# Kernel tuning notes

Measured on AMD Instinct MI355X. Metric: run time of the kernel, lower is better.

## Reference

```python
import jax, jax.numpy as jnp
import numpy as np

NUM_Q, NUM_P = 8192, 4096


def setup_inputs() -> dict:
    key = jax.random.key(0)
    k1, k2 = jax.random.split(key)
    pred = jax.random.normal(k1, (NUM_Q, NUM_P), dtype=jnp.float32)
    y = jax.random.randint(k2, (NUM_Q, NUM_P), 0, 2, dtype=jnp.int32)
    # guarantee every query has at least one relevant passage (argwhere(y==1) nonempty)
    y = y.at[:, 0].set(1)
    return {"pred": pred, "y": y}


def reference(pred, y):
    # Per row: comparer = min of pred over relevant (y==1) entries.
    # MarginRankingLoss(margin=0, reduction='mean') with target=(y!=1):
    #   target==1 (non-relevant): max(0, -(comparer - pred_j)) = relu(pred_j - min_rlv)
    #   target==0 (relevant):     max(0, 0) = 0
    rlv = (y == 1)
    min_rlv = jnp.min(jnp.where(rlv, pred, jnp.inf), axis=1, keepdims=True)  # [Q,1]
    hinge = jnp.where(rlv, 0.0, jnp.maximum(pred - min_rlv, 0.0))            # [Q,P]
    per_q = hinge.mean(axis=1)                                               # [Q]
    return per_q.mean()
```

## Files before the change

kernel.cpp:

```cpp
#include <hip/hip_runtime.h>
#include <float.h>

#define NUM_Q 8192
#define NUM_P 4096

typedef float  f32x4 __attribute__((ext_vector_type(4)));
typedef int    i32x4 __attribute__((ext_vector_type(4)));

__global__ __launch_bounds__(256)
void mmrl_kernel(const float* __restrict__ pred,
                 const int* __restrict__ y,
                 float* __restrict__ ws) {
    const int row = blockIdx.x;
    const int t = threadIdx.x;

    const f32x4* prow = reinterpret_cast<const f32x4*>(pred + (size_t)row * NUM_P);
    const i32x4* yrow = reinterpret_cast<const i32x4*>(y + (size_t)row * NUM_P);

    i32x4 yv[4];
#pragma unroll
    for (int i = 0; i < 4; ++i) yv[i] = __builtin_nontemporal_load(&yrow[t + 256 * i]);
    f32x4 pv[4];
#pragma unroll
    for (int i = 0; i < 4; ++i) pv[i] = __builtin_nontemporal_load(&prow[t + 256 * i]);

    unsigned int m = 0u;
#pragma unroll
    for (int i = 0; i < 4; ++i) {
        m |= ((unsigned int)(yv[i].x == 1)      ) << (4 * i);
        m |= ((unsigned int)(yv[i].y == 1) << 1 ) << (4 * i);
        m |= ((unsigned int)(yv[i].z == 1) << 2 ) << (4 * i);
        m |= ((unsigned int)(yv[i].w == 1) << 3 ) << (4 * i);
    }

    float lmin = FLT_MAX;
#pragma unroll
    for (int i = 0; i < 4; ++i) {
        lmin = fminf(lmin, (m & (1u << (4 * i)))     ? pv[i].x : FLT_MAX);
        lmin = fminf(lmin, (m & (2u << (4 * i)))     ? pv[i].y : FLT_MAX);
        lmin = fminf(lmin, (m & (4u << (4 * i)))     ? pv[i].z : FLT_MAX);
        lmin = fminf(lmin, (m & (8u << (4 * i)))     ? pv[i].w : FLT_MAX);
    }
#pragma unroll
    for (int off = 32; off > 0; off >>= 1)
        lmin = fminf(lmin, __shfl_xor(lmin, off));

    __shared__ float smin[4];
    __shared__ float ssum[4];
    const int wave = t >> 6;
    if ((t & 63) == 0) smin[wave] = lmin;
    __syncthreads();
    const float rmin = fminf(fminf(smin[0], smin[1]), fminf(smin[2], smin[3]));

    float lsum = 0.0f;
#pragma unroll
    for (int i = 0; i < 4; ++i) {
        lsum += (m & (1u << (4 * i))) ? 0.0f : fmaxf(pv[i].x - rmin, 0.0f);
        lsum += (m & (2u << (4 * i))) ? 0.0f : fmaxf(pv[i].y - rmin, 0.0f);
        lsum += (m & (4u << (4 * i))) ? 0.0f : fmaxf(pv[i].z - rmin, 0.0f);
        lsum += (m & (8u << (4 * i))) ? 0.0f : fmaxf(pv[i].w - rmin, 0.0f);
    }
#pragma unroll
    for (int off = 32; off > 0; off >>= 1)
        lsum += __shfl_xor(lsum, off);

    if ((t & 63) == 0) ssum[wave] = lsum;
    __syncthreads();

    if (t == 0) {
        ws[row] = (ssum[0] + ssum[1]) + (ssum[2] + ssum[3]);
    }
}

__global__ __launch_bounds__(256)
void mmrl_reduce_kernel(const float* __restrict__ partial,
                        float* __restrict__ out) {
    const int t = threadIdx.x;
    const f32x4* p4 = reinterpret_cast<const f32x4*>(partial);
    float s = 0.0f;
#pragma unroll
    for (int i = 0; i < 8; ++i) {
        f32x4 v = p4[t + 256 * i];
        s += (v.x + v.y) + (v.z + v.w);
    }
#pragma unroll
    for (int off = 32; off > 0; off >>= 1)
        s += __shfl_xor(s, off);

    __shared__ float ss[4];
    if ((t & 63) == 0) ss[t >> 6] = s;
    __syncthreads();

    if (t == 0) {
        const float total = (ss[0] + ss[1]) + (ss[2] + ss[3]);
        out[0] = total * (1.0f / ((float)NUM_Q * (float)NUM_P));
    }
}

extern "C" void kernel_launch(void* const* d_in, const int* in_sizes, int n_in,
                              void* d_out, int out_size, void* d_ws, size_t ws_size,
                              hipStream_t stream) {
    const float* pred = (const float*)d_in[0];
    const int*   y    = (const int*)d_in[1];
    float* out = (float*)d_out;
    float* ws  = (float*)d_ws;

    mmrl_kernel<<<NUM_Q, 256, 0, stream>>>(pred, y, ws);
    mmrl_reduce_kernel<<<1, 256, 0, stream>>>(ws, out);
}
```

Measured before the change: 249.5 us.

## Process two rows per block and write per-wave partial sums

```diff
diff --git a/kernel.cpp b/kernel.cpp
--- a/kernel.cpp
+++ b/kernel.cpp
@@ -11,64 +11,83 @@
 void mmrl_kernel(const float* __restrict__ pred,
                  const int* __restrict__ y,
                  float* __restrict__ ws) {
-    const int row = blockIdx.x;
-    const int t = threadIdx.x;
+    const int row0 = blockIdx.x * 2;
+    const int t    = threadIdx.x;
+    const int wave = t >> 6;
+    const int lane = t & 63;
 
-    const f32x4* prow = reinterpret_cast<const f32x4*>(pred + (size_t)row * NUM_P);
-    const i32x4* yrow = reinterpret_cast<const i32x4*>(y + (size_t)row * NUM_P);
+    const f32x4* p0 = reinterpret_cast<const f32x4*>(pred + (size_t)row0 * NUM_P);
+    const i32x4* y0 = reinterpret_cast<const i32x4*>(y    + (size_t)row0 * NUM_P);
 
-    i32x4 yv[4];
+    i32x4 yv[8];
 #pragma unroll
-    for (int i = 0; i < 4; ++i) yv[i] = __builtin_nontemporal_load(&yrow[t + 256 * i]);
-    f32x4 pv[4];
+    for (int i = 0; i < 4; ++i) yv[i]     = __builtin_nontemporal_load(&y0[t + 256 * i]);
 #pragma unroll
-    for (int i = 0; i < 4; ++i) pv[i] = __builtin_nontemporal_load(&prow[t + 256 * i]);
+    for (int i = 0; i < 4; ++i) yv[4 + i] = __builtin_nontemporal_load(&y0[1024 + t + 256 * i]);
+    f32x4 pv[8];
+#pragma unroll
+    for (int i = 0; i < 4; ++i) pv[i]     = __builtin_nontemporal_load(&p0[t + 256 * i]);
+#pragma unroll
+    for (int i = 0; i < 4; ++i) pv[4 + i] = __builtin_nontemporal_load(&p0[1024 + t + 256 * i]);
 
-    unsigned int m = 0u;
+    unsigned int m0 = 0u, m1 = 0u;
 #pragma unroll
     for (int i = 0; i < 4; ++i) {
-        m |= ((unsigned int)(yv[i].x == 1)      ) << (4 * i);
-        m |= ((unsigned int)(yv[i].y == 1) << 1 ) << (4 * i);
-        m |= ((unsigned int)(yv[i].z == 1) << 2 ) << (4 * i);
-        m |= ((unsigned int)(yv[i].w == 1) << 3 ) << (4 * i);
+        m0 |= ((unsigned int)(yv[i].x == 1)     ) << (4 * i);
+        m0 |= ((unsigned int)(yv[i].y == 1) << 1) << (4 * i);
+        m0 |= ((unsigned int)(yv[i].z == 1) << 2) << (4 * i);
+        m0 |= ((unsigned int)(yv[i].w == 1) << 3) << (4 * i);
+        m1 |= ((unsigned int)(yv[4 + i].x == 1)     ) << (4 * i);
+        m1 |= ((unsigned int)(yv[4 + i].y == 1) << 1) << (4 * i);
+        m1 |= ((unsigned int)(yv[4 + i].z == 1) << 2) << (4 * i);
+        m1 |= ((unsigned int)(yv[4 + i].w == 1) << 3) << (4 * i);
     }
 
-    float lmin = FLT_MAX;
+    float lmin0 = FLT_MAX, lmin1 = FLT_MAX;
 #pragma unroll
     for (int i = 0; i < 4; ++i) {
-        lmin = fminf(lmin, (m & (1u << (4 * i)))     ? pv[i].x : FLT_MAX);
-        lmin = fminf(lmin, (m & (2u << (4 * i)))     ? pv[i].y : FLT_MAX);
-        lmin = fminf(lmin, (m & (4u << (4 * i)))     ? pv[i].z : FLT_MAX);
-        lmin = fminf(lmin, (m & (8u << (4 * i)))     ? pv[i].w : FLT_MAX);
+        lmin0 = fminf(lmin0, (m0 & (1u << (4 * i))) ? pv[i].x : FLT_MAX);
+        lmin0 = fminf(lmin0, (m0 & (2u << (4 * i))) ? pv[i].y : FLT_MAX);
+        lmin0 = fminf(lmin0, (m0 & (4u << (4 * i))) ? pv[i].z : FLT_MAX);
+        lmin0 = fminf(lmin0, (m0 & (8u << (4 * i))) ? pv[i].w : FLT_MAX);
+        lmin1 = fminf(lmin1, (m1 & (1u << (4 * i))) ? pv[4 + i].x : FLT_MAX);
+        lmin1 = fminf(lmin1, (m1 & (2u << (4 * i))) ? pv[4 + i].y : FLT_MAX);
+        lmin1 = fminf(lmin1, (m1 & (4u << (4 * i))) ? pv[4 + i].z : FLT_MAX);
+        lmin1 = fminf(lmin1, (m1 & (8u << (4 * i))) ? pv[4 + i].w : FLT_MAX);
     }
 #pragma unroll
-    for (int off = 32; off > 0; off >>= 1)
-        lmin = fminf(lmin, __shfl_xor(lmin, off));
+    for (int off = 32; off > 0; off >>= 1) {
+        lmin0 = fminf(lmin0, __shfl_xor(lmin0, off));
+        lmin1 = fminf(lmin1, __shfl_xor(lmin1, off));
+    }
 
-    __shared__ float smin[4];
-    __shared__ float ssum[4];
-    const int wave = t >> 6;
-    if ((t & 63) == 0) smin[wave] = lmin;
+    __shared__ float smin[2][4];
+    if (lane == 0) { smin[0][wave] = lmin0; smin[1][wave] = lmin1; }
     __syncthreads();
-    const float rmin = fminf(fminf(smin[0], smin[1]), fminf(smin[2], smin[3]));
+    const float rmin0 = fminf(fminf(smin[0][0], smin[0][1]), fminf(smin[0][2], smin[0][3]));
+    const float rmin1 = fminf(fminf(smin[1][0], smin[1][1]), fminf(smin[1][2], smin[1][3]));
 
-    float lsum = 0.0f;
+    float lsum0 = 0.0f, lsum1 = 0.0f;
 #pragma unroll
     for (int i = 0; i < 4; ++i) {
-        lsum += (m & (1u << (4 * i))) ? 0.0f : fmaxf(pv[i].x - rmin, 0.0f);
-        lsum += (m & (2u << (4 * i))) ? 0.0f : fmaxf(pv[i].y - rmin, 0.0f);
-        lsum += (m & (4u << (4 * i))) ? 0.0f : fmaxf(pv[i].z - rmin, 0.0f);
-        lsum += (m & (8u << (4 * i))) ? 0.0f : fmaxf(pv[i].w - rmin, 0.0f);
+        lsum0 += (m0 & (1u << (4 * i))) ? 0.0f : fmaxf(pv[i].x - rmin0, 0.0f);
+        lsum0 += (m0 & (2u << (4 * i))) ? 0.0f : fmaxf(pv[i].y - rmin0, 0.0f);
+        lsum0 += (m0 & (4u << (4 * i))) ? 0.0f : fmaxf(pv[i].z - rmin0, 0.0f);
+        lsum0 += (m0 & (8u << (4 * i))) ? 0.0f : fmaxf(pv[i].w - rmin0, 0.0f);
+        lsum1 += (m1 & (1u << (4 * i))) ? 0.0f : fmaxf(pv[4 + i].x - rmin1, 0.0f);
+        lsum1 += (m1 & (2u << (4 * i))) ? 0.0f : fmaxf(pv[4 + i].y - rmin1, 0.0f);
+        lsum1 += (m1 & (4u << (4 * i))) ? 0.0f : fmaxf(pv[4 + i].z - rmin1, 0.0f);
+        lsum1 += (m1 & (8u << (4 * i))) ? 0.0f : fmaxf(pv[4 + i].w - rmin1, 0.0f);
     }
 #pragma unroll
-    for (int off = 32; off > 0; off >>= 1)
-        lsum += __shfl_xor(lsum, off);
+    for (int off = 32; off > 0; off >>= 1) {
+        lsum0 += __shfl_xor(lsum0, off);
+        lsum1 += __shfl_xor(lsum1, off);
+    }
 
-    if ((t & 63) == 0) ssum[wave] = lsum;
-    __syncthreads();
-
-    if (t == 0) {
-        ws[row] = (ssum[0] + ssum[1]) + (ssum[2] + ssum[3]);
+    if (lane == 0) {
+        ws[(size_t)row0 * 4 + wave]       = lsum0;
+        ws[(size_t)(row0 + 1) * 4 + wave] = lsum1;
     }
 }
 
@@ -79,7 +98,7 @@
     const f32x4* p4 = reinterpret_cast<const f32x4*>(partial);
     float s = 0.0f;
 #pragma unroll
-    for (int i = 0; i < 8; ++i) {
+    for (int i = 0; i < 32; ++i) {
         f32x4 v = p4[t + 256 * i];
         s += (v.x + v.y) + (v.z + v.w);
     }
@@ -105,6 +124,6 @@
     float* out = (float*)d_out;
     float* ws  = (float*)d_ws;
 
-    mmrl_kernel<<<NUM_Q, 256, 0, stream>>>(pred, y, ws);
+    mmrl_kernel<<<NUM_Q / 2, 256, 0, stream>>>(pred, y, ws);
     mmrl_reduce_kernel<<<1, 256, 0, stream>>>(ws, out);
 }
```

Measured after the change: 250.8 us. About the same (+0.5%).

## Process four rows per block with software-prefetch of next row

Applied to the files above, without the earlier changes.

```diff
diff --git a/kernel.cpp b/kernel.cpp
--- a/kernel.cpp
+++ b/kernel.cpp
@@ -3,72 +3,94 @@
 
 #define NUM_Q 8192
 #define NUM_P 4096
+#define ROWS  4
+#define VEC   (NUM_P / 4)
 
 typedef float  f32x4 __attribute__((ext_vector_type(4)));
 typedef int    i32x4 __attribute__((ext_vector_type(4)));
+
+__device__ __forceinline__ unsigned mask_of(const i32x4* yv) {
+    unsigned m = 0u;
+#pragma unroll
+    for (int i = 0; i < 4; ++i) {
+        m |= ((unsigned)(yv[i].x == 1)     ) << (4 * i);
+        m |= ((unsigned)(yv[i].y == 1) << 1) << (4 * i);
+        m |= ((unsigned)(yv[i].z == 1) << 2) << (4 * i);
+        m |= ((unsigned)(yv[i].w == 1) << 3) << (4 * i);
+    }
+    return m;
+}
 
 __global__ __launch_bounds__(256)
 void mmrl_kernel(const float* __restrict__ pred,
                  const int* __restrict__ y,
                  float* __restrict__ ws) {
-    const int row = blockIdx.x;
-    const int t = threadIdx.x;
+    const int t    = threadIdx.x;
+    const int wave = t >> 6;
+    const int lane = t & 63;
+    const int row0 = blockIdx.x * ROWS;
 
-    const f32x4* prow = reinterpret_cast<const f32x4*>(pred + (size_t)row * NUM_P);
-    const i32x4* yrow = reinterpret_cast<const i32x4*>(y + (size_t)row * NUM_P);
+    const f32x4* P = reinterpret_cast<const f32x4*>(pred) + (size_t)row0 * VEC;
+    const i32x4* Y = reinterpret_cast<const i32x4*>(y)    + (size_t)row0 * VEC;
+
+    __shared__ float smin[2][4];
 
     i32x4 yv[4];
+    f32x4 pv[4], nv[4];
+
 #pragma unroll
-    for (int i = 0; i < 4; ++i) yv[i] = __builtin_nontemporal_load(&yrow[t + 256 * i]);
-    f32x4 pv[4];
+    for (int i = 0; i < 4; ++i) yv[i] = __builtin_nontemporal_load(&Y[t + 256 * i]);
 #pragma unroll
-    for (int i = 0; i < 4; ++i) pv[i] = __builtin_nontemporal_load(&prow[t + 256 * i]);
+    for (int i = 0; i < 4; ++i) pv[i] = __builtin_nontemporal_load(&P[t + 256 * i]);
+    unsigned m = mask_of(yv);
 
-    unsigned int m = 0u;
 #pragma unroll
-    for (int i = 0; i < 4; ++i) {
-        m |= ((unsigned int)(yv[i].x == 1)      ) << (4 * i);
-        m |= ((unsigned int)(yv[i].y == 1) << 1 ) << (4 * i);
-        m |= ((unsigned int)(yv[i].z == 1) << 2 ) << (4 * i);
-        m |= ((unsigned int)(yv[i].w == 1) << 3 ) << (4 * i);
-    }
+    for (int r = 0; r < ROWS; ++r) {
+        if (r + 1 < ROWS) {
+            const size_t base = (size_t)(r + 1) * VEC + t;
+#pragma unroll
+            for (int i = 0; i < 4; ++i) yv[i] = __builtin_nontemporal_load(&Y[base + 256 * i]);
+#pragma unroll
+            for (int i = 0; i < 4; ++i) nv[i] = __builtin_nontemporal_load(&P[base + 256 * i]);
+        }
 
-    float lmin = FLT_MAX;
+        float lmin = FLT_MAX;
 #pragma unroll
-    for (int i = 0; i < 4; ++i) {
-        lmin = fminf(lmin, (m & (1u << (4 * i)))     ? pv[i].x : FLT_MAX);
-        lmin = fminf(lmin, (m & (2u << (4 * i)))     ? pv[i].y : FLT_MAX);
-        lmin = fminf(lmin, (m & (4u << (4 * i)))     ? pv[i].z : FLT_MAX);
-        lmin = fminf(lmin, (m & (8u << (4 * i)))     ? pv[i].w : FLT_MAX);
-    }
+        for (int i = 0; i < 4; ++i) {
+            lmin = fminf(lmin, (m & (1u << (4 * i))) ? pv[i].x : FLT_MAX);
+            lmin = fminf(lmin, (m & (2u << (4 * i))) ? pv[i].y : FLT_MAX);
+            lmin = fminf(lmin, (m & (4u << (4 * i))) ? pv[i].z : FLT_MAX);
+            lmin = fminf(lmin, (m & (8u << (4 * i))) ? pv[i].w : FLT_MAX);
+        }
 #pragma unroll
-    for (int off = 32; off > 0; off >>= 1)
-        lmin = fminf(lmin, __shfl_xor(lmin, off));
+        for (int off = 32; off > 0; off >>= 1)
+            lmin = fminf(lmin, __shfl_xor(lmin, off));
 
-    __shared__ float smin[4];
-    __shared__ float ssum[4];
-    const int wave = t >> 6;
-    if ((t & 63) == 0) smin[wave] = lmin;
-    __syncthreads();
-    const float rmin = fminf(fminf(smin[0], smin[1]), fminf(smin[2], smin[3]));
+        if (lane == 0) smin[r & 1][wave] = lmin;
+        asm volatile("s_waitcnt lgkmcnt(0)" ::: "memory");
+        __builtin_amdgcn_s_barrier();
+        const float rmin = fminf(fminf(smin[r & 1][0], smin[r & 1][1]),
+                                 fminf(smin[r & 1][2], smin[r & 1][3]));
 
-    float lsum = 0.0f;
+        float lsum = 0.0f;
 #pragma unroll
-    for (int i = 0; i < 4; ++i) {
-        lsum += (m & (1u << (4 * i))) ? 0.0f : fmaxf(pv[i].x - rmin, 0.0f);
-        lsum += (m & (2u << (4 * i))) ? 0.0f : fmaxf(pv[i].y - rmin, 0.0f);
-        lsum += (m & (4u << (4 * i))) ? 0.0f : fmaxf(pv[i].z - rmin, 0.0f);
-        lsum += (m & (8u << (4 * i))) ? 0.0f : fmaxf(pv[i].w - rmin, 0.0f);
-    }
+        for (int i = 0; i < 4; ++i) {
+            lsum += (m & (1u << (4 * i))) ? 0.0f : fmaxf(pv[i].x - rmin, 0.0f);
+            lsum += (m & (2u << (4 * i))) ? 0.0f : fmaxf(pv[i].y - rmin, 0.0f);
+            lsum += (m & (4u << (4 * i))) ? 0.0f : fmaxf(pv[i].z - rmin, 0.0f);
+            lsum += (m & (8u << (4 * i))) ? 0.0f : fmaxf(pv[i].w - rmin, 0.0f);
+        }
 #pragma unroll
-    for (int off = 32; off > 0; off >>= 1)
-        lsum += __shfl_xor(lsum, off);
+        for (int off = 32; off > 0; off >>= 1)
+            lsum += __shfl_xor(lsum, off);
 
-    if ((t & 63) == 0) ssum[wave] = lsum;
-    __syncthreads();
+        if (lane == 0) ws[(size_t)(row0 + r) * 4 + wave] = lsum;
 
-    if (t == 0) {
-        ws[row] = (ssum[0] + ssum[1]) + (ssum[2] + ssum[3]);
+        if (r + 1 < ROWS) {
+            m = mask_of(yv);
+#pragma unroll
+            for (int i = 0; i < 4; ++i) pv[i] = nv[i];
+        }
     }
 }
 
@@ -79,7 +101,7 @@
     const f32x4* p4 = reinterpret_cast<const f32x4*>(partial);
     float s = 0.0f;
 #pragma unroll
-    for (int i = 0; i < 8; ++i) {
+    for (int i = 0; i < 32; ++i) {
         f32x4 v = p4[t + 256 * i];
         s += (v.x + v.y) + (v.z + v.w);
     }
@@ -105,6 +127,6 @@
     float* out = (float*)d_out;
     float* ws  = (float*)d_ws;
 
-    mmrl_kernel<<<NUM_Q, 256, 0, stream>>>(pred, y, ws);
+    mmrl_kernel<<<NUM_Q / ROWS, 256, 0, stream>>>(pred, y, ws);
     mmrl_reduce_kernel<<<1, 256, 0, stream>>>(ws, out);
 }
```

After: 251.1 us. About the same (+0.6%).
